# Optimization experiments

Measured on AMD Instinct MI355X. Metric: run time of the kernel, lower is better.

## Reference

```python
import jax, jax.numpy as jnp
import numpy as np

C = 256
CQK = C // 8  # reduction_ratio = 8


def setup_inputs() -> dict:
    key = jax.random.key(0)
    ks = jax.random.split(key, 8)
    B, H, W = 8, 64, 64
    x = jax.random.normal(ks[0], (B, C, H, W), dtype=jnp.float32)
    s_in = 1.0 / np.sqrt(C)
    Wq = jax.random.normal(ks[1], (CQK, C), dtype=jnp.float32) * s_in
    bq = jax.random.normal(ks[2], (CQK,), dtype=jnp.float32) * 0.01
    Wk = jax.random.normal(ks[3], (CQK, C), dtype=jnp.float32) * s_in
    bk = jax.random.normal(ks[4], (CQK,), dtype=jnp.float32) * 0.01
    Wv = jax.random.normal(ks[5], (C, C), dtype=jnp.float32) * s_in
    bv = jax.random.normal(ks[6], (C,), dtype=jnp.float32) * 0.01
    gamma = jax.random.normal(ks[7], (1,), dtype=jnp.float32) * 0.1
    return {"x": x, "Wq": Wq, "bq": bq, "Wk": Wk, "bk": bk,
            "Wv": Wv, "bv": bv, "gamma": gamma}


def reference(x, Wq, bq, Wk, bk, Wv, bv, gamma):
    B, Cc, H, W = x.shape
    N = H * W
    xf = x.reshape(B, Cc, N)  # [B, C, N]
    # 1x1 convs == per-pixel linear maps over channels
    q = jnp.einsum('qc,bcn->bnq', Wq, xf) + bq            # [B, N, Cqk]
    k = jnp.einsum('kc,bcn->bkn', Wk, xf) + bk[None, :, None]  # [B, Cqk, N]
    v = jnp.einsum('vc,bcn->bvn', Wv, xf) + bv[None, :, None]  # [B, C, N]
    # unscaled attention scores, softmax over keys (last dim)
    scores = jax.nn.softmax(jnp.einsum('bnq,bqm->bnm', q, k), axis=-1)  # [B, N, N]
    # out[b,c,n] = sum_m v[b,c,m] * scores[b,n,m]  (torch: value @ scores^T)
    attn = jnp.einsum('bvm,bnm->bvn', v, scores)          # [B, C, N]
    out = gamma[0] * attn.reshape(B, Cc, H, W) + x
    return out
```

## Files before the change

kernel.cpp:

```cpp
#include <hip/hip_runtime.h>

static constexpr int B_   = 8;
static constexpr int C_   = 256;
static constexpr int CQK_ = 32;
static constexpr int N_   = 4096;

typedef __attribute__((ext_vector_type(4))) float f32x4;
typedef __attribute__((ext_vector_type(8))) short short8;
typedef __attribute__((ext_vector_type(2))) unsigned int u32x2;
typedef unsigned short ushort_t;

__device__ inline unsigned short f2bf(float f) {
    unsigned u = __float_as_uint(f);
    return (unsigned short)((u + 0x7FFFu + ((u >> 16) & 1u)) >> 16);
}
__device__ inline unsigned packbf(float lo, float hi) {
    return (unsigned)f2bf(lo) | ((unsigned)f2bf(hi) << 16);
}

__device__ inline int swzbits(int m) {
    return ((m & 3) << 5) | (((m >> 3) & 1) << 4);
}

template <int OFF>
__device__ inline u32x2 tr8(unsigned a) {
    u32x2 d;
    asm volatile("ds_read_b64_tr_b16 %0, %1 offset:%2"
                 : "=v"(d) : "v"(a), "i"(OFF));
    return d;
}

__device__ inline short8 mk8(u32x2 lo, u32x2 hi) {
    union { unsigned u[4]; short8 s; } v;
    v.u[0] = lo.x; v.u[1] = lo.y; v.u[2] = hi.x; v.u[3] = hi.y;
    return v.s;
}

__global__ __launch_bounds__(256) void prep_kernel(
    const float* __restrict__ Wq, const float* __restrict__ bq,
    const float* __restrict__ Wk, const float* __restrict__ bk,
    const float* __restrict__ Wv, const float* __restrict__ bv,
    ushort_t* __restrict__ Wall, float* __restrict__ ball)
{
    const int r = blockIdx.x;
    const int t = threadIdx.x;
    const float* src;
    float bsrc;
    if (r < 32)      { src = Wq + (size_t)r * C_;        bsrc = bq[r]; }
    else if (r < 64) { src = Wk + (size_t)(r - 32) * C_; bsrc = bk[r - 32]; }
    else             { src = Wv + (size_t)(r - 64) * C_; bsrc = bv[r - 64]; }
    Wall[(size_t)r * C_ + t] = f2bf(src[t]);
    if (t == 0) ball[r] = bsrc;
}

__global__ __launch_bounds__(256) void proj_kernel(
    const float* __restrict__ x,
    const ushort_t* __restrict__ Wall, const float* __restrict__ ball,
    ushort_t* __restrict__ Qb, ushort_t* __restrict__ Kb, ushort_t* __restrict__ Vt)
{
    __shared__ __align__(16) unsigned char xs[C_ * 128];
    typedef __attribute__((address_space(3))) unsigned char lds_byte;
    const unsigned sbase = (unsigned)(size_t)(lds_byte*)xs;

    const int b  = blockIdx.x & 7;
    const int n0 = (blockIdx.x >> 3) << 6;
    const int t  = threadIdx.x;

    {
        const int cst = t >> 4;
        const int n4  = (t & 15) << 2;
        const float* xb = x + (size_t)b * C_ * N_ + n0;
        #pragma unroll
        for (int i = 0; i < 16; ++i) {
            const int c = 16 * i + cst;
            float4 v = *(const float4*)(xb + (size_t)c * N_ + n4);
            u32x2 pk;
            pk.x = packbf(v.x, v.y);
            pk.y = packbf(v.z, v.w);
            *(u32x2*)(xs + c * 128 + ((n4 * 2) ^ swzbits(c))) = pk;
        }
    }
    __syncthreads();

    const int l  = t & 63, w = t >> 6;
    const int li = l & 15, g = l >> 4;
    const int rr = li >> 2, ss = l & 3;
    const int swz_tr = (rr << 5) | ((g & 1) << 4);

    f32x4 acc[5][4];
    #pragma unroll
    for (int i = 0; i < 5; ++i)
        #pragma unroll
        for (int j = 0; j < 4; ++j) acc[i][j] = (f32x4){0.f, 0.f, 0.f, 0.f};

    #pragma unroll 2
    for (int kg = 0; kg < 8; ++kg) {
        u32x2 pb[4][2];
        #pragma unroll
        for (int jn = 0; jn < 4; ++jn) {
            unsigned a = sbase + (32 * kg + 8 * g + rr) * 128
                       + ((32 * jn + 8 * ss) ^ swz_tr);
            pb[jn][0] = tr8<0>(a);
            pb[jn][1] = tr8<512>(a);
        }
        short8 af[5];
        #pragma unroll
        for (int tm = 0; tm < 5; ++tm)
            af[tm] = *(const short8*)(Wall + (size_t)(16 * (4 * tm + w) + li) * C_
                                      + 32 * kg + 8 * g);
        asm volatile("s_waitcnt lgkmcnt(0)" ::: "memory");
        __builtin_amdgcn_sched_barrier(0);
        #pragma unroll
        for (int jn = 0; jn < 4; ++jn) {
            short8 Bf = mk8(pb[jn][0], pb[jn][1]);
            acc[0][jn] = __builtin_amdgcn_mfma_f32_16x16x32_bf16(
                             af[0], Bf, acc[0][jn], 0, 0, 0);
            #pragma unroll
            for (int tm = 1; tm < 5; ++tm)
                acc[tm][jn] = __builtin_amdgcn_mfma_f32_16x16x32_bf16(
                                  Bf, af[tm], acc[tm][jn], 0, 0, 0);
        }
    }

    {
        const int oc0 = 16 * w + 4 * g;
        float4 bias = *(const float4*)(ball + oc0);
        ushort_t* dst = (w < 2) ? Qb : Kb;
        const int col = (w < 2) ? oc0 : (oc0 - 32);
        #pragma unroll
        for (int jn = 0; jn < 4; ++jn) {
            const int n = n0 + 16 * jn + li;
            f32x4 a = acc[0][jn];
            u32x2 pk;
            pk.x = packbf(a[0] + bias.x, a[1] + bias.y);
            pk.y = packbf(a[2] + bias.z, a[3] + bias.w);
            *(u32x2*)(dst + (size_t)(b * N_ + n) * CQK_ + col) = pk;
        }
    }
    {
        const int sx = (li & 7) << 4;
        #pragma unroll
        for (int tm = 1; tm < 5; ++tm) {
            const int c  = 16 * (4 * tm + w) + li - 64;
            const float bc = ball[64 + c];
            char* vrow = (char*)Vt
                       + ((size_t)(b * 64 + (n0 >> 6)) * 256 + c) * 128;
            #pragma unroll
            for (int jn = 0; jn < 4; ++jn) {
                f32x4 a = acc[tm][jn];
                u32x2 pk;
                pk.x = packbf(a[0] + bc, a[1] + bc);
                pk.y = packbf(a[2] + bc, a[3] + bc);
                *(u32x2*)(vrow + ((32 * jn + 8 * g) ^ sx)) = pk;
            }
        }
    }
}

__global__ __launch_bounds__(256) void attn_kernel(
    const float* __restrict__ x,
    const ushort_t* __restrict__ Qb, const ushort_t* __restrict__ Kb,
    const ushort_t* __restrict__ Vt,
    const float* __restrict__ gamma, float* __restrict__ out)
{
    __shared__ __align__(16) unsigned char smem[81920];

    const int b  = blockIdx.x & 7;
    const int n0 = (blockIdx.x >> 3) << 6;
    const int t  = threadIdx.x;
    const int l  = t & 63, w = t >> 6;
    const int li = l & 15, g = l >> 4;
    const int hq = w & 1,  hc = w >> 1;
    const int sx = (li & 7) << 4;
    unsigned char* Pw = smem + 65536 + w * 4096;

    short8 qf[2];
    #pragma unroll
    for (int jq = 0; jq < 2; ++jq)
        qf[jq] = *(const short8*)(Qb + (size_t)(b * N_ + n0 + 32 * hq + 16 * jq + li) * CQK_ + 8 * g);

    f32x4 acc[2][8];
    #pragma unroll
    for (int i = 0; i < 2; ++i)
        #pragma unroll
        for (int j = 0; j < 8; ++j) acc[i][j] = (f32x4){0.f, 0.f, 0.f, 0.f};
    float rs[2] = {0.f, 0.f};

    const ushort_t* Kbb = Kb + (size_t)(b * N_) * CQK_;
    const char* Vtb = (const char*)Vt + (size_t)b * 64 * 32768;
    const f32x4 zf = {0.f, 0.f, 0.f, 0.f};

    short8 kfA[4], kfB[4];

    {
        const char* gsrc = Vtb + t * 16;
        #pragma unroll
        for (int i = 0; i < 8; ++i)
            __builtin_amdgcn_global_load_lds(
                (const __attribute__((address_space(1))) unsigned int*)(gsrc + i * 4096),
                (__attribute__((address_space(3))) unsigned int*)(smem + t * 16 + i * 4096),
                16, 0, 0);
        #pragma unroll
        for (int jm = 0; jm < 4; ++jm)
            kfA[jm] = *(const short8*)(Kbb + (size_t)(16 * jm + li) * CQK_ + 8 * g);
    }
    asm volatile("s_waitcnt vmcnt(0)" ::: "memory");
    __syncthreads();

#define CHUNK_BODY(MC, BUFR, BUFW, KFC, KFN)                                    \
    {                                                                           \
        const int mcn = ((MC) + 1) & 63;                                        \
                       \
        const char* gsrc = Vtb + (size_t)mcn * 32768 + t * 16;                  \
        _Pragma("unroll")                                                       \
        for (int i = 0; i < 8; ++i)                                             \
            __builtin_amdgcn_global_load_lds(                                   \
                (const __attribute__((address_space(1))) unsigned int*)(gsrc + i * 4096), \
                (__attribute__((address_space(3))) unsigned int*)((BUFW) + t * 16 + i * 4096), \
                16, 0, 0);                                                      \
                                    \
        _Pragma("unroll")                                                       \
        for (int jm = 0; jm < 4; ++jm)                                          \
            KFN[jm] = *(const short8*)(Kbb + (size_t)(64 * mcn + 16 * jm + li) * CQK_ + 8 * g); \
                               \
        _Pragma("unroll")                                                       \
        for (int jm = 0; jm < 4; ++jm) {                                        \
            _Pragma("unroll")                                                   \
            for (int jq = 0; jq < 2; ++jq) {                                    \
                f32x4 s = __builtin_amdgcn_mfma_f32_16x16x32_bf16(              \
                              KFC[jm], qf[jq], zf, 0, 0, 0);                    \
                float e0 = __expf(s[0]), e1 = __expf(s[1]);                     \
                float e2 = __expf(s[2]), e3 = __expf(s[3]);                     \
                rs[jq] += (e0 + e1) + (e2 + e3);                                \
                u32x2 pk; pk.x = packbf(e0, e1); pk.y = packbf(e2, e3);         \
                *(u32x2*)(Pw + (16 * jq + li) * 128                             \
                             + ((32 * jm + 8 * g) ^ sx)) = pk;                  \
            }                                                                   \
        }                                                                       \
        asm volatile("s_waitcnt lgkmcnt(0)" ::: "memory");                      \
        __builtin_amdgcn_sched_barrier(0);                                      \
              \
        _Pragma("unroll")                                                       \
        for (int kb = 0; kb < 2; ++kb) {                                        \
            short8 pa[2], vb[8];                                                \
            _Pragma("unroll")                                                   \
            for (int jq = 0; jq < 2; ++jq)                                      \
                pa[jq] = *(const short8*)(Pw + (16 * jq + li) * 128             \
                                             + ((64 * kb + 16 * g) ^ sx));      \
            _Pragma("unroll")                                                   \
            for (int jc = 0; jc < 8; ++jc)                                      \
                vb[jc] = *(const short8*)((BUFR)                                \
                             + (128 * hc + 16 * jc + li) * 128                  \
                             + ((64 * kb + 16 * g) ^ sx));                      \
            _Pragma("unroll")                                                   \
            for (int jq = 0; jq < 2; ++jq)                                      \
                _Pragma("unroll")                                               \
                for (int jc = 0; jc < 8; ++jc)                                  \
                    acc[jq][jc] = __builtin_amdgcn_mfma_f32_16x16x32_bf16(      \
                                      pa[jq], vb[jc], acc[jq][jc], 0, 0, 0);    \
        }                                                                       \
                            \
        asm volatile("s_waitcnt vmcnt(0)" ::: "memory");                        \
        __syncthreads();                                                        \
    }

    for (int mc = 0; mc < 64; mc += 2) {
        CHUNK_BODY(mc,     smem,         smem + 32768, kfA, kfB)
        CHUNK_BODY(mc + 1, smem + 32768, smem,         kfB, kfA)
    }
#undef CHUNK_BODY

    #pragma unroll
    for (int jq = 0; jq < 2; ++jq) {
        rs[jq] += __shfl_xor(rs[jq], 16, 64);
        rs[jq] += __shfl_xor(rs[jq], 32, 64);
    }
    float inv[2][4];
    #pragma unroll
    for (int jq = 0; jq < 2; ++jq)
        #pragma unroll
        for (int r = 0; r < 4; ++r) {
            int v = __builtin_amdgcn_ds_bpermute((4 * g + r) * 4,
                                                 __float_as_int(rs[jq]));
            inv[jq][r] = 1.0f / __int_as_float(v);
        }

    const float gm = gamma[0];
    #pragma unroll
    for (int jq = 0; jq < 2; ++jq)
        #pragma unroll
        for (int jc = 0; jc < 8; ++jc) {
            const int c = 128 * hc + 16 * jc + li;
            const size_t rowoff = (size_t)(b * C_ + c) * N_
                                + n0 + 32 * hq + 16 * jq + 4 * g;
            float4 xv = *(const float4*)(x + rowoff);
            f32x4 a = acc[jq][jc];
            float4 o;
            o.x = gm * a[0] * inv[jq][0] + xv.x;
            o.y = gm * a[1] * inv[jq][1] + xv.y;
            o.z = gm * a[2] * inv[jq][2] + xv.z;
            o.w = gm * a[3] * inv[jq][3] + xv.w;
            *(float4*)(out + rowoff) = o;
        }
}

extern "C" void kernel_launch(void* const* d_in, const int* in_sizes, int n_in,
                              void* d_out, int out_size, void* d_ws, size_t ws_size,
                              hipStream_t stream)
{
    const float* x     = (const float*)d_in[0];
    const float* Wq    = (const float*)d_in[1];
    const float* bq    = (const float*)d_in[2];
    const float* Wk    = (const float*)d_in[3];
    const float* bk    = (const float*)d_in[4];
    const float* Wv    = (const float*)d_in[5];
    const float* bv    = (const float*)d_in[6];
    const float* gamma = (const float*)d_in[7];
    float* out = (float*)d_out;

    ushort_t* ws = (ushort_t*)d_ws;
    ushort_t* Qb   = ws;
    ushort_t* Kb   = Qb + (size_t)B_ * N_ * CQK_;
    ushort_t* Vt   = Kb + (size_t)B_ * N_ * CQK_;
    ushort_t* Wall = Vt + (size_t)B_ * C_ * N_;
    float*    ball = (float*)(Wall + (size_t)320 * C_);

    prep_kernel<<<320, 256, 0, stream>>>(Wq, bq, Wk, bk, Wv, bv, Wall, ball);
    proj_kernel<<<B_ * (N_ / 64), 256, 0, stream>>>(x, Wall, ball, Qb, Kb, Vt);
    attn_kernel<<<B_ * (N_ / 64), 256, 0, stream>>>(x, Qb, Kb, Vt, gamma, out);
}
```

Measured before the change: 159.2 us.

## Deepen V/K prefetch to two chunks ahead with partial vmcnt waits

The attention loop now keeps two V chunks in flight: it loads chunks 0 and 1 up front and, after each chunk's PV MFMAs, refills the buffer just consumed with chunk mc+2. A partial vmcnt wait replaces the full drain, so global loads overlap more compute. The softmax exponent switches to exp2f, with log2(e) folded into the Q weights and bias in the prep kernel, and bf16 packing uses the hardware v_cvt_pk_bf16_f32 instruction. The vmcnt(12) count and the raw s_barrier ordering are fragile and depend on the exact number of outstanding loads; bf16 rounding of Q weights scaled by log2(e) shifts the numerics slightly.

Result: slower. 231.6 us (+45.4%).

```diff
diff --git a/kernel.cpp b/kernel.cpp
--- a/kernel.cpp
+++ b/kernel.cpp
@@ -16,6 +16,11 @@
 }
 __device__ inline unsigned packbf(float lo, float hi) {
     return (unsigned)f2bf(lo) | ((unsigned)f2bf(hi) << 16);
+}
+__device__ inline unsigned cvtpk(float lo, float hi) {
+    unsigned r;
+    asm("v_cvt_pk_bf16_f32 %0, %1, %2" : "=v"(r) : "v"(lo), "v"(hi));
+    return r;
 }
 
 __device__ inline int swzbits(int m) {
@@ -44,13 +49,14 @@
 {
     const int r = blockIdx.x;
     const int t = threadIdx.x;
+    const float LOG2E = 1.4426950408889634f;
     const float* src;
-    float bsrc;
-    if (r < 32)      { src = Wq + (size_t)r * C_;        bsrc = bq[r]; }
-    else if (r < 64) { src = Wk + (size_t)(r - 32) * C_; bsrc = bk[r - 32]; }
-    else             { src = Wv + (size_t)(r - 64) * C_; bsrc = bv[r - 64]; }
-    Wall[(size_t)r * C_ + t] = f2bf(src[t]);
-    if (t == 0) ball[r] = bsrc;
+    float bsrc, sc;
+    if (r < 32)      { src = Wq + (size_t)r * C_;        bsrc = bq[r];      sc = LOG2E; }
+    else if (r < 64) { src = Wk + (size_t)(r - 32) * C_; bsrc = bk[r - 32]; sc = 1.0f; }
+    else             { src = Wv + (size_t)(r - 64) * C_; bsrc = bv[r - 64]; sc = 1.0f; }
+    Wall[(size_t)r * C_ + t] = f2bf(src[t] * sc);
+    if (t == 0) ball[r] = bsrc * sc;
 }
 
 __global__ __launch_bounds__(256) void proj_kernel(
@@ -192,54 +198,57 @@
 
     short8 kfA[4], kfB[4];
 
+    #pragma unroll
+    for (int jm = 0; jm < 4; ++jm) {
+        kfA[jm] = *(const short8*)(Kbb + (size_t)(16 * jm + li) * CQK_ + 8 * g);
+        kfB[jm] = *(const short8*)(Kbb + (size_t)(64 + 16 * jm + li) * CQK_ + 8 * g);
+    }
     {
         const char* gsrc = Vtb + t * 16;
         #pragma unroll
-        for (int i = 0; i < 8; ++i)
+        for (int i = 0; i < 8; ++i) {
             __builtin_amdgcn_global_load_lds(
                 (const __attribute__((address_space(1))) unsigned int*)(gsrc + i * 4096),
                 (__attribute__((address_space(3))) unsigned int*)(smem + t * 16 + i * 4096),
                 16, 0, 0);
-        #pragma unroll
-        for (int jm = 0; jm < 4; ++jm)
-            kfA[jm] = *(const short8*)(Kbb + (size_t)(16 * jm + li) * CQK_ + 8 * g);
-    }
-    asm volatile("s_waitcnt vmcnt(0)" ::: "memory");
-    __syncthreads();
-
-#define CHUNK_BODY(MC, BUFR, BUFW, KFC, KFN)                                    \
+            __builtin_amdgcn_global_load_lds(
+                (const __attribute__((address_space(1))) unsigned int*)(gsrc + 32768 + i * 4096),
+                (__attribute__((address_space(3))) unsigned int*)(smem + 32768 + t * 16 + i * 4096),
+                16, 0, 0);
+        }
+    }
+
+#define CHUNK_BODY(MC, BUFR, KFC)                                               \
     {                                                                           \
-        const int mcn = ((MC) + 1) & 63;                                        \
-                       \
-        const char* gsrc = Vtb + (size_t)mcn * 32768 + t * 16;                  \
-        _Pragma("unroll")                                                       \
-        for (int i = 0; i < 8; ++i)                                             \
-            __builtin_amdgcn_global_load_lds(                                   \
-                (const __attribute__((address_space(1))) unsigned int*)(gsrc + i * 4096), \
-                (__attribute__((address_space(3))) unsigned int*)((BUFW) + t * 16 + i * 4096), \
-                16, 0, 0);                                                      \
-                                    \
-        _Pragma("unroll")                                                       \
-        for (int jm = 0; jm < 4; ++jm)                                          \
-            KFN[jm] = *(const short8*)(Kbb + (size_t)(64 * mcn + 16 * jm + li) * CQK_ + 8 * g); \
-                               \
+           \
         _Pragma("unroll")                                                       \
         for (int jm = 0; jm < 4; ++jm) {                                        \
             _Pragma("unroll")                                                   \
             for (int jq = 0; jq < 2; ++jq) {                                    \
                 f32x4 s = __builtin_amdgcn_mfma_f32_16x16x32_bf16(              \
                               KFC[jm], qf[jq], zf, 0, 0, 0);                    \
-                float e0 = __expf(s[0]), e1 = __expf(s[1]);                     \
-                float e2 = __expf(s[2]), e3 = __expf(s[3]);                     \
+                float e0 = exp2f(s[0]), e1 = exp2f(s[1]);                       \
+                float e2 = exp2f(s[2]), e3 = exp2f(s[3]);                       \
                 rs[jq] += (e0 + e1) + (e2 + e3);                                \
-                u32x2 pk; pk.x = packbf(e0, e1); pk.y = packbf(e2, e3);         \
+                u32x2 pk; pk.x = cvtpk(e0, e1); pk.y = cvtpk(e2, e3);           \
                 *(u32x2*)(Pw + (16 * jq + li) * 128                             \
                              + ((32 * jm + 8 * g) ^ sx)) = pk;                  \
             }                                                                   \
         }                                                                       \
-        asm volatile("s_waitcnt lgkmcnt(0)" ::: "memory");                      \
+                         \
+        {                                                                       \
+            const int mk = ((MC) + 2) & 63;                                     \
+            _Pragma("unroll")                                                   \
+            for (int jm = 0; jm < 4; ++jm)                                      \
+                KFC[jm] = *(const short8*)(Kbb                                  \
+                    + (size_t)(64 * mk + 16 * jm + li) * CQK_ + 8 * g);         \
+        }                                                                       \
+          \
+                    \
+        asm volatile("s_waitcnt vmcnt(12)" ::: "memory");                       \
+        __builtin_amdgcn_s_barrier();                                           \
         __builtin_amdgcn_sched_barrier(0);                                      \
-              \
+                         \
         _Pragma("unroll")                                                       \
         for (int kb = 0; kb < 2; ++kb) {                                        \
             short8 pa[2], vb[8];                                                \
@@ -259,14 +268,26 @@
                     acc[jq][jc] = __builtin_amdgcn_mfma_f32_16x16x32_bf16(      \
                                       pa[jq], vb[jc], acc[jq][jc], 0, 0, 0);    \
         }                                                                       \
-                            \
-        asm volatile("s_waitcnt vmcnt(0)" ::: "memory");                        \
-        __syncthreads();                                                        \
+              \
+        asm volatile("s_waitcnt lgkmcnt(0)" ::: "memory");                      \
+        __builtin_amdgcn_s_barrier();                                           \
+        __builtin_amdgcn_sched_barrier(0);                                      \
+                 \
+        {                                                                       \
+            const int mv = ((MC) + 2) & 63;                                     \
+            const char* gsrc = Vtb + (size_t)mv * 32768 + t * 16;               \
+            _Pragma("unroll")                                                   \
+            for (int i = 0; i < 8; ++i)                                         \
+                __builtin_amdgcn_global_load_lds(                               \
+                    (const __attribute__((address_space(1))) unsigned int*)(gsrc + i * 4096), \
+                    (__attribute__((address_space(3))) unsigned int*)((BUFR) + t * 16 + i * 4096), \
+                    16, 0, 0);                                                  \
+        }                                                                       \
     }
 
     for (int mc = 0; mc < 64; mc += 2) {
-        CHUNK_BODY(mc,     smem,         smem + 32768, kfA, kfB)
-        CHUNK_BODY(mc + 1, smem + 32768, smem,         kfB, kfA)
+        CHUNK_BODY(mc,     smem,         kfA)
+        CHUNK_BODY(mc + 1, smem + 32768, kfB)
     }
 #undef CHUNK_BODY
 
```
